# Kernel optimization log

Hardware: AMD Instinct MI355X
Metric: run time of the kernel (lower is better)

## Reference

```python
import jax, jax.numpy as jnp
import numpy as np

N_QUBITS = 20
BATCH = 16


def setup_inputs() -> dict:
    key = jax.random.key(0)
    k1, k2 = jax.random.split(key)
    phi = jax.random.normal(k1, (BATCH, 2 ** N_QUBITS), dtype=jnp.float32)
    thetas = jax.random.normal(k2, (BATCH, N_QUBITS), dtype=jnp.float32)
    return {"phi": phi, "thetas": thetas}


def reference(phi, thetas):
    """Apply per-qubit RX(theta) rotations to the state vector.

    phi: [B, 2**n] real float32 initial amplitudes (cast to complex64).
    thetas: [B, n] rotation angles, qubit 0 = most-significant bit
    (matches torch view([B] + [2]*n) axis ordering, applied sequentially).
    Returns real/imag stacked: [B, 2**n, 2] float32.
    """
    B, S = phi.shape
    n = N_QUBITS
    c = jnp.cos(thetas / 2).astype(jnp.complex64)          # [B, n]
    s = (-1j * jnp.sin(thetas / 2)).astype(jnp.complex64)  # [B, n]
    state = phi.astype(jnp.complex64)                      # [B, S]
    for i in range(n):  # fixed small loop over qubits (butterfly stages)
        left = 2 ** i
        right = S // (2 * left)
        st = state.reshape(B, left, 2, right)
        a = st[:, :, 0, :]
        b = st[:, :, 1, :]
        ci = c[:, i, None, None]
        si = s[:, i, None, None]
        na = ci * a + si * b
        nb = si * a + ci * b
        state = jnp.stack([na, nb], axis=2).reshape(B, S)
    return jnp.stack([state.real, state.imag], axis=-1)
```

## Files before the change

kernel.cpp:

```cpp
#include <hip/hip_runtime.h>

#define NQ 20

__device__ __forceinline__ float bcast_first(float x) {
    return __int_as_float(__builtin_amdgcn_readfirstlane(__float_as_int(x)));
}

__device__ __forceinline__ void bfly(float C, float SV, float2& a, float2& b) {
    float2 na = make_float2(C * a.x + SV * b.y, C * a.y - SV * b.x);
    float2 nb = make_float2(C * b.x + SV * a.y, C * b.y - SV * a.x);
    a = na; b = nb;
}

__device__ __forceinline__ void bfly4(float C, float SV, float4& a, float4& b) {
    float4 na = make_float4(C*a.x + SV*b.y, C*a.y - SV*b.x, C*a.z + SV*b.w, C*a.w - SV*b.z);
    float4 nb = make_float4(C*b.x + SV*a.y, C*b.y - SV*a.x, C*b.z + SV*a.w, C*b.w - SV*a.z);
    a = na; b = nb;
}

__device__ __forceinline__ int swz1(int l) { return l ^ (((l >> 7) & 7) << 2); }

__global__ __launch_bounds__(64) void rx_pass1(
        const float* __restrict__ phi, const float* __restrict__ thetas,
        float2* __restrict__ out) {
    __shared__ float2 lds[2048];
    const int lane = threadIdx.x;
    const int W = blockIdx.x;
    const int b = W >> 9;
    const int base = (W & 511) << 11;
    const float* ph = phi + ((size_t)b << NQ) + base;
    float2* op = out + ((size_t)b << NQ) + base;

    float c[11], sv[11];
#pragma unroll
    for (int beta = 0; beta < 11; ++beta) {
        float th = 0.5f * thetas[b * NQ + (NQ - 1 - beta)];
        c[beta]  = bcast_first(cosf(th));
        sv[beta] = bcast_first(sinf(th));
    }

    float2 v[32];
#pragma unroll
    for (int k4 = 0; k4 < 8; ++k4) {
        float4 t = *(const float4*)(ph + (k4 << 8) + (lane << 2));
        v[k4 * 4 + 0] = make_float2(t.x, 0.f);
        v[k4 * 4 + 1] = make_float2(t.y, 0.f);
        v[k4 * 4 + 2] = make_float2(t.z, 0.f);
        v[k4 * 4 + 3] = make_float2(t.w, 0.f);
    }

    const int regbit1[5]  = {0, 1, 8, 9, 10};
    const int regmask1[5] = {1, 2, 4, 8, 16};
#pragma unroll
    for (int t = 0; t < 5; ++t) {
        const float C = c[regbit1[t]], SV = sv[regbit1[t]];
        const int m = regmask1[t];
#pragma unroll
        for (int r = 0; r < 32; ++r)
            if (!(r & m)) bfly(C, SV, v[r], v[r | m]);
    }

#pragma unroll
    for (int k4 = 0; k4 < 8; ++k4) {
        int low0 = (k4 << 8) + (lane << 2);
        int s0 = swz1(low0);
        *(float4*)&lds[s0]     = make_float4(v[k4*4+0].x, v[k4*4+0].y, v[k4*4+1].x, v[k4*4+1].y);
        *(float4*)&lds[s0 + 2] = make_float4(v[k4*4+2].x, v[k4*4+2].y, v[k4*4+3].x, v[k4*4+3].y);
    }
    __syncthreads();

    {
        const int g = lane >> 2, lam = lane & 3;
        float2 w2[32];
#pragma unroll
        for (int r = 0; r < 32; ++r) {
            int l = (g << 7) | (r << 2) | lam;
            w2[r] = lds[swz1(l)];
        }
#pragma unroll
        for (int t = 0; t < 5; ++t) {
            const float C = c[2 + t], SV = sv[2 + t];
            const int m = 1 << t;
#pragma unroll
            for (int r = 0; r < 32; ++r)
                if (!(r & m)) bfly(C, SV, w2[r], w2[r | m]);
        }
#pragma unroll
        for (int r = 0; r < 32; ++r) {
            int l = (g << 7) | (r << 2) | lam;
            lds[swz1(l)] = w2[r];
        }
    }
    __syncthreads();

    float4 u[16];
#pragma unroll
    for (int m = 0; m < 16; ++m) {
        int l0 = (lane << 1) | ((m & 1) << 7) | (((m >> 1) & 1) << 8)
               | (((m >> 2) & 1) << 9) | (((m >> 3) & 1) << 10);
        u[m] = *(float4*)&lds[swz1(l0)];
    }
    {
        const float C = c[7], SV = sv[7];
#pragma unroll
        for (int m = 0; m < 16; m += 2) {
            float4 A = u[m], B = u[m + 1];
            u[m]     = make_float4(C*A.x + SV*B.y, C*A.y - SV*B.x, C*A.z + SV*B.w, C*A.w - SV*B.z);
            u[m + 1] = make_float4(C*B.x + SV*A.y, C*B.y - SV*A.x, C*B.z + SV*A.w, C*B.w - SV*A.z);
        }
    }
#pragma unroll
    for (int m = 0; m < 16; ++m) {
        int l0 = (lane << 1) | ((m & 1) << 7) | (((m >> 1) & 1) << 8)
               | (((m >> 2) & 1) << 9) | (((m >> 3) & 1) << 10);
        *(float4*)(op + l0) = u[m];
    }
}

__device__ __forceinline__ int ppos(int h, int q) {
    return (h << 4) + (((q ^ (h & 7) ^ ((h >> 5) & 7)) & 7) << 1);
}

__global__ __launch_bounds__(256) void rx_pass2(
        const float* __restrict__ thetas, float2* __restrict__ out) {
    __shared__ float2 buf[8192];
    const int tid = threadIdx.x;
    const int b = blockIdx.x >> 7;
    const int lb = blockIdx.x & 127;
    float2* p = out + ((size_t)b << NQ) + (lb << 4);

    float c[9], sv[9];
#pragma unroll
    for (int i = 0; i < 9; ++i) {
        float th = 0.5f * thetas[b * NQ + (8 - i)];
        c[i]  = bcast_first(cosf(th));
        sv[i] = bcast_first(sinf(th));
    }

#pragma unroll
    for (int i = 0; i < 16; ++i) {
        int f = (i << 8) | tid;
        int h = f >> 3, j = f & 7;
        float4 t = *(const float4*)(p + h * 2048 + (j << 1));
        *(float4*)&buf[ppos(h, j)] = t;
    }
    __syncthreads();

    {
        const int hl = tid & 31;
        const int j  = tid >> 5;
        float4 w[16];
#pragma unroll
        for (int m = 0; m < 16; ++m)
            w[m] = *(float4*)&buf[ppos((m << 5) | hl, j)];
#pragma unroll
        for (int t = 0; t < 4; ++t) {
            const float C = c[5 + t], SV = sv[5 + t];
            const int msk = 1 << t;
#pragma unroll
            for (int m = 0; m < 16; ++m)
                if (!(m & msk)) bfly4(C, SV, w[m], w[m | msk]);
        }
#pragma unroll
        for (int m = 0; m < 16; ++m)
            *(float4*)&buf[ppos((m << 5) | hl, j)] = w[m];
    }
    __syncthreads();

    {
        const int hh = tid >> 4;
        const int ll = tid & 15;
        float2 v[32];
#pragma unroll
        for (int r = 0; r < 32; ++r) {
            int h = (hh << 5) | r;
            v[r] = buf[ppos(h, ll >> 1) + (ll & 1)];
        }
#pragma unroll
        for (int t = 0; t < 5; ++t) {
            const float C = c[t], SV = sv[t];
            const int msk = 1 << t;
#pragma unroll
            for (int r = 0; r < 32; ++r)
                if (!(r & msk)) bfly(C, SV, v[r], v[r | msk]);
        }
#pragma unroll
        for (int r = 0; r < 32; ++r) {
            int h = (hh << 5) | r;
            p[h * 2048 + ll] = v[r];
        }
    }
}

extern "C" void kernel_launch(void* const* d_in, const int* in_sizes, int n_in,
                              void* d_out, int out_size, void* d_ws, size_t ws_size,
                              hipStream_t stream) {
    const float* phi    = (const float*)d_in[0];
    const float* thetas = (const float*)d_in[1];
    float2* out = (float2*)d_out;
    rx_pass1<<<8192, 64, 0, stream>>>(phi, thetas, out);
    rx_pass2<<<2048, 256, 0, stream>>>(thetas, out);
}
```

Baseline: 239.7 us.

## Store pass-1 intermediate state as fp16 in workspace to halve traffic

Pass 1 now writes its intermediate complex amplitudes as half2 into the workspace instead of float2 into the output. A new pass 2 reads that half-precision buffer, computes in fp32, and writes the final fp32 output. It also processes 32 columns per block with half the block count. The aim is to cut the intermediate write and read bandwidth in half, at the cost of fp16 rounding error on the intermediate state, which may exceed tolerance. The old fp32 path is kept as a fallback when the workspace is too small.

After: 258.6 us. 1.08x slower.

```diff
diff --git a/kernel.cpp b/kernel.cpp
--- a/kernel.cpp
+++ b/kernel.cpp
@@ -1,4 +1,5 @@
 #include <hip/hip_runtime.h>
+#include <hip/hip_fp16.h>
 
 #define NQ 20
 
@@ -18,18 +19,32 @@
     a = na; b = nb;
 }
 
+__device__ __forceinline__ float4 h4_to_f4(float2 raw) {
+    __half2* h = (__half2*)&raw;
+    float2 a = __half22float2(h[0]);
+    float2 b = __half22float2(h[1]);
+    return make_float4(a.x, a.y, b.x, b.y);
+}
+__device__ __forceinline__ float2 f4_to_h4(float4 v) {
+    float2 r;
+    __half2* h = (__half2*)&r;
+    h[0] = __float22half2_rn(make_float2(v.x, v.y));
+    h[1] = __float22half2_rn(make_float2(v.z, v.w));
+    return r;
+}
+
 __device__ __forceinline__ int swz1(int l) { return l ^ (((l >> 7) & 7) << 2); }
 
+template <bool FP16>
 __global__ __launch_bounds__(64) void rx_pass1(
         const float* __restrict__ phi, const float* __restrict__ thetas,
-        float2* __restrict__ out) {
+        float2* __restrict__ out, __half2* __restrict__ inter) {
     __shared__ float2 lds[2048];
     const int lane = threadIdx.x;
     const int W = blockIdx.x;
     const int b = W >> 9;
     const int base = (W & 511) << 11;
     const float* ph = phi + ((size_t)b << NQ) + base;
-    float2* op = out + ((size_t)b << NQ) + base;
 
     float c[11], sv[11];
 #pragma unroll
@@ -109,11 +124,110 @@
             u[m + 1] = make_float4(C*B.x + SV*A.y, C*B.y - SV*A.x, C*B.z + SV*A.w, C*B.w - SV*A.z);
         }
     }
-#pragma unroll
-    for (int m = 0; m < 16; ++m) {
-        int l0 = (lane << 1) | ((m & 1) << 7) | (((m >> 1) & 1) << 8)
-               | (((m >> 2) & 1) << 9) | (((m >> 3) & 1) << 10);
-        *(float4*)(op + l0) = u[m];
+    if (FP16) {
+        __half2* ip = inter + ((size_t)b << NQ) + base;
+#pragma unroll
+        for (int m = 0; m < 16; ++m) {
+            int l0 = (lane << 1) | ((m & 1) << 7) | (((m >> 1) & 1) << 8)
+                   | (((m >> 2) & 1) << 9) | (((m >> 3) & 1) << 10);
+            *(float2*)&ip[l0] = f4_to_h4(u[m]);
+        }
+    } else {
+        float2* op = out + ((size_t)b << NQ) + base;
+#pragma unroll
+        for (int m = 0; m < 16; ++m) {
+            int l0 = (lane << 1) | ((m & 1) << 7) | (((m >> 1) & 1) << 8)
+                   | (((m >> 2) & 1) << 9) | (((m >> 3) & 1) << 10);
+            *(float4*)(op + l0) = u[m];
+        }
+    }
+}
+
+__global__ __launch_bounds__(256) void rx_pass2_h(
+        const float* __restrict__ thetas, const __half2* __restrict__ ws,
+        float2* __restrict__ out) {
+    __shared__ __half2 buf[16384];
+    const int tid = threadIdx.x;
+    const int b = blockIdx.x >> 6;
+    const int lb = blockIdx.x & 63;
+    const __half2* pin = ws + ((size_t)b << NQ) + (lb << 5);
+    float2* pout = out + ((size_t)b << NQ) + (lb << 5);
+
+    float c[9], sv[9];
+#pragma unroll
+    for (int i = 0; i < 9; ++i) {
+        float th = 0.5f * thetas[b * NQ + (8 - i)];
+        c[i]  = bcast_first(cosf(th));
+        sv[i] = bcast_first(sinf(th));
+    }
+
+#pragma unroll
+    for (int i = 0; i < 16; ++i) {
+        int f = (i << 8) | tid;
+        int h = f >> 3, j = f & 7;
+        float4 t = *(const float4*)&pin[h * 2048 + (j << 2)];
+        *(float4*)&buf[(h << 5) + ((j ^ (h & 7)) << 2)] = t;
+    }
+    __syncthreads();
+
+    {
+        const int hl = tid & 31;
+        const int j  = tid >> 5;
+        float4 wa[16], wb[16];
+#pragma unroll
+        for (int m = 0; m < 16; ++m) {
+            int h = (m << 5) | hl;
+            float4 V = *(float4*)&buf[(h << 5) + ((j ^ (h & 7)) << 2)];
+            float2* half_pair = (float2*)&V;
+            wa[m] = h4_to_f4(half_pair[0]);
+            wb[m] = h4_to_f4(half_pair[1]);
+        }
+#pragma unroll
+        for (int t = 0; t < 4; ++t) {
+            const float C = c[5 + t], SV = sv[5 + t];
+            const int msk = 1 << t;
+#pragma unroll
+            for (int m = 0; m < 16; ++m)
+                if (!(m & msk)) {
+                    bfly4(C, SV, wa[m], wa[m | msk]);
+                    bfly4(C, SV, wb[m], wb[m | msk]);
+                }
+        }
+#pragma unroll
+        for (int m = 0; m < 16; ++m) {
+            int h = (m << 5) | hl;
+            float4 V;
+            float2* half_pair = (float2*)&V;
+            half_pair[0] = f4_to_h4(wa[m]);
+            half_pair[1] = f4_to_h4(wb[m]);
+            *(float4*)&buf[(h << 5) + ((j ^ (h & 7)) << 2)] = V;
+        }
+    }
+    __syncthreads();
+
+    {
+        const int hh = tid >> 4;
+        const int lp = tid & 15;
+        float4 v[32];
+#pragma unroll
+        for (int r = 0; r < 32; ++r) {
+            int h = (hh << 5) | r;
+            float2 d = *(float2*)&buf[(h << 5) + (((lp >> 1) ^ (h & 7)) << 2) + ((lp & 1) << 1)];
+            v[r] = h4_to_f4(d);
+        }
+#pragma unroll
+        for (int t = 0; t < 5; ++t) {
+            const float C = c[t], SV = sv[t];
+            const int msk = 1 << t;
+#pragma unroll
+            for (int r = 0; r < 32; ++r)
+                if (!(r & msk)) bfly4(C, SV, v[r], v[r | msk]);
+        }
+#pragma unroll
+        for (int r = 0; r < 32; ++r) {
+            int h = (hh << 5) | r;
+            *(float4*)&pout[h * 2048 + (lp << 1)] = v[r];
+        }
     }
 }
 
@@ -121,7 +235,7 @@
     return (h << 4) + (((q ^ (h & 7) ^ ((h >> 5) & 7)) & 7) << 1);
 }
 
-__global__ __launch_bounds__(256) void rx_pass2(
+__global__ __launch_bounds__(256) void rx_pass2_f(
         const float* __restrict__ thetas, float2* __restrict__ out) {
     __shared__ float2 buf[8192];
     const int tid = threadIdx.x;
@@ -198,6 +312,13 @@
     const float* phi    = (const float*)d_in[0];
     const float* thetas = (const float*)d_in[1];
     float2* out = (float2*)d_out;
-    rx_pass1<<<8192, 64, 0, stream>>>(phi, thetas, out);
-    rx_pass2<<<2048, 256, 0, stream>>>(thetas, out);
-}
+    const size_t need = (size_t)16 * (1u << NQ) * sizeof(__half2);
+    if (ws_size >= need) {
+        __half2* inter = (__half2*)d_ws;
+        rx_pass1<true><<<8192, 64, 0, stream>>>(phi, thetas, out, inter);
+        rx_pass2_h<<<1024, 256, 0, stream>>>(thetas, inter, out);
+    } else {
+        rx_pass1<false><<<8192, 64, 0, stream>>>(phi, thetas, out, nullptr);
+        rx_pass2_f<<<2048, 256, 0, stream>>>(thetas, out);
+    }
+}
```
